# Kernel optimization log

Measured on AMD Instinct MI355X. Metric: run time of the kernel, lower is better.

Reference implementation:

```python
import jax, jax.numpy as jnp
import numpy as np
from jax import lax

PATCH = 16
TAU = 0.5
EPS = 1e-8  # torch CosineSimilarity default eps


def setup_inputs() -> dict:
    key = jax.random.key(0)
    k1, k2, k3, k4, k5 = jax.random.split(key, 5)
    B, C, HW = 64, 3, 384
    hidden, latent = 768, 1024
    return {
        "x": jax.random.normal(k1, (B, C, HW, HW), dtype=jnp.float32),
        "conv_w": jax.random.normal(k2, (hidden, C, PATCH, PATCH), dtype=jnp.float32) * 0.02,
        "conv_b": jax.random.normal(k3, (hidden,), dtype=jnp.float32) * 0.02,
        "latent1": jax.random.normal(k4, (1, latent, hidden), dtype=jnp.float32),
        "latent2": jax.random.normal(k5, (1, latent, hidden), dtype=jnp.float32),
    }


def _cosine_scores(p, p_norm, lat):
    # p: (B, N, D); lat: (L, D) -> (B, N, L) cosine similarity
    l_norm = jnp.linalg.norm(lat, axis=-1)  # (L,)
    dots = jnp.einsum('bnd,ld->bnl', p, lat)
    denom = jnp.maximum(p_norm[:, :, None] * l_norm[None, None, :], EPS)
    return dots / denom


def reference(x, conv_w, conv_b, latent1, latent2):
    # Patch embedding: Conv2d(kernel=stride=16, padding=0)
    patch = lax.conv_general_dilated(
        x, conv_w, window_strides=(PATCH, PATCH), padding='VALID',
        dimension_numbers=('NCHW', 'OIHW', 'NCHW'))
    patch = patch + conv_b[None, :, None, None]  # (B, D, H', W')
    B, D = patch.shape[0], patch.shape[1]
    p = patch.reshape(B, D, -1).transpose(0, 2, 1)  # (B, N, D)
    p_norm = jnp.linalg.norm(p, axis=-1)  # (B, N)

    far = _cosine_scores(p, p_norm, latent1[0])    # (B, N, L)
    close = _cosine_scores(p, p_norm, latent2[0])  # (B, N, L)

    sum_close = jnp.sum(jnp.exp(close / TAU), axis=(1, 2))  # (B,)
    sum_far = jnp.sum(jnp.exp(far / TAU), axis=(1, 2))      # (B,)
    loss = -jnp.log(sum_close / sum_far)
    return loss.mean()
```

## Files before the change

kernel.cpp:

```cpp
#include <hip/hip_runtime.h>
#include <math.h>

using f32x4  = __attribute__((ext_vector_type(4))) float;
using bf16x8 = __attribute__((ext_vector_type(8))) short;

typedef const __attribute__((address_space(1))) void gas_void;
typedef __attribute__((address_space(3))) void las_void;

__device__ __forceinline__ void gl16(const void* g, void* l) {
    __builtin_amdgcn_global_load_lds((gas_void*)g, (las_void*)l, 16, 0, 0);
}

__device__ __forceinline__ unsigned short f2bf(float f) {
    union { float f; unsigned u; } v; v.f = f;
    unsigned r = v.u + 0x7fffu + ((v.u >> 16) & 1u);
    return (unsigned short)(r >> 16);
}
__device__ __forceinline__ float bf2f(unsigned short u) {
    return __uint_as_float(((unsigned)u) << 16);
}

#define VW0() asm volatile("s_waitcnt vmcnt(0)")
#define VWL0() asm volatile("s_waitcnt vmcnt(0) lgkmcnt(0)")
#define BAR() __builtin_amdgcn_s_barrier()

__global__ void pcl_prep_wl(const float* __restrict__ w,
                            const float* __restrict__ l1, const float* __restrict__ l2,
                            unsigned short* __restrict__ wsW,
                            unsigned short* __restrict__ wsL) {
    int r = blockIdx.x, t = threadIdx.x;
    if (r < 768) {
        const float* src = w + (size_t)r * 768;
        unsigned short* dst = wsW + (size_t)r * 768;
#pragma unroll
        for (int i = 0; i < 12; ++i) dst[t + 64 * i] = f2bf(src[t + 64 * i]);
    } else {
        int lr = r - 768;
        const float* src = (lr < 1024) ? l1 + (size_t)lr * 768 : l2 + (size_t)(lr - 1024) * 768;
        unsigned short* dst = wsL + (size_t)lr * 768;
        float vals[12];
        float s = 0.f;
#pragma unroll
        for (int i = 0; i < 12; ++i) {
            float f = bf2f(f2bf(src[t + 64 * i]));
            vals[i] = f; s += f * f;
        }
#pragma unroll
        for (int off = 32; off; off >>= 1) s += __shfl_xor(s, off, 64);
        float rn = 1.0f / sqrtf(s);
#pragma unroll
        for (int i = 0; i < 12; ++i) dst[t + 64 * i] = f2bf(vals[i] * rn);
    }
}

#define K1_LDS 81920

__global__ __launch_bounds__(256, 2)
void pcl_k1(const float* __restrict__ x,
            const unsigned short* __restrict__ wsW,
            const float* __restrict__ bias,
            unsigned short* __restrict__ pbuf,
            float* __restrict__ rpnp) {
    extern __shared__ char smem[];
    const int t = threadIdx.x, w = t >> 6, l = t & 63;
    const int wg = (blockIdx.x & 7) * 144 + (blockIdx.x >> 3);
    const int mt = wg / 6, nt = wg % 6;
    const size_t Mb = (size_t)mt * 192;
    const int Nb = nt * 128;
    const int wm = w >> 1, wn = w & 1;
    const int ir = l >> 3, s2 = (l & 7) ^ ir;
    const int lm = l & 15, lg4 = l >> 4;

    char* buf0 = smem;
    char* buf1 = smem + 40960;

    const int sl8 = t & 7;
    const float* xbase[6];
    int awoff[6];
#pragma unroll
    for (int rep = 0; rep < 6; ++rep) {
        int row = rep * 32 + (t >> 3);
        int n = (int)Mb + row;
        int b = n / 576, n5 = n % 576;
        int ph = n5 / 24, pw = n5 % 24;
        xbase[rep] = x + (size_t)b * 442368 + (size_t)ph * 6144 + pw * 16;
        awoff[rep] = row * 128 + ((sl8 ^ (row & 7)) << 4);
    }
    auto xoff = [&](int kt) {
        int k0 = kt * 64 + sl8 * 8;
        return (k0 >> 8) * 147456 + (((k0 >> 4) & 15)) * 384 + (k0 & 15);
    };

    auto issueB = [&](int kt, char* buf) {
#pragma unroll
        for (int rr = 0; rr < 4; ++rr) {
            int c2 = w * 4 + rr;
            gl16(wsW + (size_t)(Nb + c2 * 8 + ir) * 768 + kt * 64 + s2 * 8,
                 buf + 24576 + c2 * 1024);
        }
    };

    f32x4 xr[6][2];
    auto loadX = [&](int kt) {
        int off = xoff(kt);
#pragma unroll
        for (int rep = 0; rep < 6; ++rep) {
            const float* s = xbase[rep] + off;
            xr[rep][0] = *(const f32x4*)s;
            xr[rep][1] = *(const f32x4*)(s + 4);
        }
    };
    auto writeA = [&](char* buf) {
#pragma unroll
        for (int rep = 0; rep < 6; ++rep) {
            bf16x8 pkt;
#pragma unroll
            for (int j = 0; j < 4; ++j) {
                pkt[j]     = (short)f2bf(xr[rep][0][j]);
                pkt[4 + j] = (short)f2bf(xr[rep][1][j]);
            }
            *(bf16x8*)(buf + awoff[rep]) = pkt;
        }
    };

    f32x4 acc[6][4];
#pragma unroll
    for (int m = 0; m < 6; ++m)
#pragma unroll
        for (int nb = 0; nb < 4; ++nb) acc[m][nb] = (f32x4)0.f;

    loadX(0);
    issueB(0, buf0);
    writeA(buf0);
    VWL0(); BAR();

    bf16x8 areg[3][2], breg[4][2];

#pragma unroll 2
    for (int kt = 0; kt < 12; ++kt) {
        char* cur = (kt & 1) ? buf1 : buf0;
        char* nxt = (kt & 1) ? buf0 : buf1;

        if (kt < 11) { loadX(kt + 1); issueB(kt + 1, nxt); }

#pragma unroll
        for (int nb = 0; nb < 4; ++nb)
#pragma unroll
            for (int ks = 0; ks < 2; ++ks) {
                int rb = wn * 64 + nb * 16 + lm, slot = ks * 4 + lg4;
                breg[nb][ks] = *(const bf16x8*)(cur + 24576 + rb * 128 + ((slot ^ (rb & 7)) << 4));
            }
#pragma unroll
        for (int m = 0; m < 3; ++m)
#pragma unroll
            for (int ks = 0; ks < 2; ++ks) {
                int r = wm * 96 + m * 16 + lm, slot = ks * 4 + lg4;
                areg[m][ks] = *(const bf16x8*)(cur + r * 128 + ((slot ^ (r & 7)) << 4));
            }
        __builtin_amdgcn_s_setprio(1);
#pragma unroll
        for (int m = 0; m < 3; ++m)
#pragma unroll
            for (int nb = 0; nb < 4; ++nb)
#pragma unroll
                for (int ks = 0; ks < 2; ++ks)
                    acc[m][nb] = __builtin_amdgcn_mfma_f32_16x16x32_bf16(areg[m][ks], breg[nb][ks], acc[m][nb], 0, 0, 0);
        __builtin_amdgcn_s_setprio(0);

#pragma unroll
        for (int m = 0; m < 3; ++m)
#pragma unroll
            for (int ks = 0; ks < 2; ++ks) {
                int r = wm * 96 + 48 + m * 16 + lm, slot = ks * 4 + lg4;
                areg[m][ks] = *(const bf16x8*)(cur + r * 128 + ((slot ^ (r & 7)) << 4));
            }
        __builtin_amdgcn_s_setprio(1);
#pragma unroll
        for (int m = 0; m < 3; ++m)
#pragma unroll
            for (int nb = 0; nb < 4; ++nb)
#pragma unroll
                for (int ks = 0; ks < 2; ++ks)
                    acc[3 + m][nb] = __builtin_amdgcn_mfma_f32_16x16x32_bf16(areg[m][ks], breg[nb][ks], acc[3 + m][nb], 0, 0, 0);
        __builtin_amdgcn_s_setprio(0);

        if (kt < 11) writeA(nxt);

        VWL0();
        BAR();
    }

    float rs[6][4];
#pragma unroll
    for (int m = 0; m < 6; ++m)
#pragma unroll
        for (int j = 0; j < 4; ++j) rs[m][j] = 0.f;
#pragma unroll
    for (int nb = 0; nb < 4; ++nb) {
        int d = Nb + wn * 64 + nb * 16 + lm;
        float bv = bias[d];
#pragma unroll
        for (int m = 0; m < 6; ++m) {
            int mh = m / 3, mi = m % 3;
#pragma unroll
            for (int j = 0; j < 4; ++j) {
                int row = wm * 96 + mh * 48 + mi * 16 + lg4 * 4 + j;
                unsigned short h = f2bf(acc[m][nb][j] + bv);
                pbuf[(Mb + row) * 768 + d] = h;
                float fv = bf2f(h);
                rs[m][j] += fv * fv;
            }
        }
    }
#pragma unroll
    for (int m = 0; m < 6; ++m)
#pragma unroll
        for (int j = 0; j < 4; ++j) {
            rs[m][j] += __shfl_xor(rs[m][j], 1);
            rs[m][j] += __shfl_xor(rs[m][j], 2);
            rs[m][j] += __shfl_xor(rs[m][j], 4);
            rs[m][j] += __shfl_xor(rs[m][j], 8);
        }
    __syncthreads();
    float* nrm = (float*)smem;
    if (lm == 0) {
#pragma unroll
        for (int m = 0; m < 6; ++m) {
            int mh = m / 3, mi = m % 3;
#pragma unroll
            for (int j = 0; j < 4; ++j) {
                int row = wm * 96 + mh * 48 + mi * 16 + lg4 * 4 + j;
                nrm[row * 2 + wn] = rs[m][j];
            }
        }
    }
    __syncthreads();
    if (t < 192) rpnp[(size_t)nt * 36864 + Mb + t] = nrm[t * 2] + nrm[t * 2 + 1];
}

__global__ void pcl_norm(const float* __restrict__ rpnp, float* __restrict__ rpn) {
    int i = blockIdx.x * 256 + threadIdx.x;
    float s = 0.f;
#pragma unroll
    for (int nt = 0; nt < 6; ++nt) s += rpnp[(size_t)nt * 36864 + i];
    rpn[i] = 1.0f / sqrtf(s);
}

#define K2_LDS 81920

__global__ __launch_bounds__(256, 2)
void pcl_k2(const unsigned short* __restrict__ pbuf,
            const unsigned short* __restrict__ wsL,
            const float* __restrict__ rpn,
            double* __restrict__ partials) {
    extern __shared__ char smem[];
    const int t = threadIdx.x, w = t >> 6, l = t & 63;
    const int wg = (blockIdx.x & 7) * 384 + (blockIdx.x >> 3);
    const int mt = wg >> 4, nt = wg & 15;
    const size_t Mb = (size_t)mt * 192;
    const int Nb = nt * 128;
    const int wm = w >> 1, wn = w & 1;
    const int ir = l >> 3, s2 = (l & 7) ^ ir;
    const int lm = l & 15, lg4 = l >> 4;

    char* buf0 = smem;
    char* buf1 = smem + 40960;

    auto stage = [&](int kt, char* buf) {
#pragma unroll
        for (int rr = 0; rr < 6; ++rr) {
            int c2 = w * 6 + rr;
            gl16(pbuf + (Mb + c2 * 8 + ir) * 768 + kt * 64 + s2 * 8, buf + c2 * 1024);
        }
#pragma unroll
        for (int rr = 0; rr < 4; ++rr) {
            int c2 = w * 4 + rr;
            gl16(wsL + (size_t)(Nb + c2 * 8 + ir) * 768 + kt * 64 + s2 * 8,
                 buf + 24576 + c2 * 1024);
        }
    };

    f32x4 acc[6][4];
#pragma unroll
    for (int m = 0; m < 6; ++m)
#pragma unroll
        for (int nb = 0; nb < 4; ++nb) acc[m][nb] = (f32x4)0.f;

    stage(0, buf0);
    VW0(); BAR();

    bf16x8 areg[3][2], breg[4][2];

#pragma unroll 2
    for (int kt = 0; kt < 12; ++kt) {
        char* cur = (kt & 1) ? buf1 : buf0;
        char* nxt = (kt & 1) ? buf0 : buf1;

        if (kt < 11) stage(kt + 1, nxt);

#pragma unroll
        for (int nb = 0; nb < 4; ++nb)
#pragma unroll
            for (int ks = 0; ks < 2; ++ks) {
                int rb = wn * 64 + nb * 16 + lm, slot = ks * 4 + lg4;
                breg[nb][ks] = *(const bf16x8*)(cur + 24576 + rb * 128 + ((slot ^ (rb & 7)) << 4));
            }
#pragma unroll
        for (int m = 0; m < 3; ++m)
#pragma unroll
            for (int ks = 0; ks < 2; ++ks) {
                int r = wm * 96 + m * 16 + lm, slot = ks * 4 + lg4;
                areg[m][ks] = *(const bf16x8*)(cur + r * 128 + ((slot ^ (r & 7)) << 4));
            }
        __builtin_amdgcn_s_setprio(1);
#pragma unroll
        for (int m = 0; m < 3; ++m)
#pragma unroll
            for (int nb = 0; nb < 4; ++nb)
#pragma unroll
                for (int ks = 0; ks < 2; ++ks)
                    acc[m][nb] = __builtin_amdgcn_mfma_f32_16x16x32_bf16(areg[m][ks], breg[nb][ks], acc[m][nb], 0, 0, 0);
        __builtin_amdgcn_s_setprio(0);

#pragma unroll
        for (int m = 0; m < 3; ++m)
#pragma unroll
            for (int ks = 0; ks < 2; ++ks) {
                int r = wm * 96 + 48 + m * 16 + lm, slot = ks * 4 + lg4;
                areg[m][ks] = *(const bf16x8*)(cur + r * 128 + ((slot ^ (r & 7)) << 4));
            }
        __builtin_amdgcn_s_setprio(1);
#pragma unroll
        for (int m = 0; m < 3; ++m)
#pragma unroll
            for (int nb = 0; nb < 4; ++nb)
#pragma unroll
                for (int ks = 0; ks < 2; ++ks)
                    acc[3 + m][nb] = __builtin_amdgcn_mfma_f32_16x16x32_bf16(areg[m][ks], breg[nb][ks], acc[3 + m][nb], 0, 0, 0);
        __builtin_amdgcn_s_setprio(0);

        VW0();
        BAR();
    }

    double ssum = 0.0;
#pragma unroll
    for (int m = 0; m < 6; ++m) {
        int mh = m / 3, mi = m % 3;
        int rl = wm * 96 + mh * 48 + mi * 16;
        float rv[4];
#pragma unroll
        for (int j = 0; j < 4; ++j) rv[j] = rpn[Mb + rl + lg4 * 4 + j];
        float es = 0.f;
#pragma unroll
        for (int nb = 0; nb < 4; ++nb)
#pragma unroll
            for (int j = 0; j < 4; ++j)
                es += __expf(2.0f * acc[m][nb][j] * rv[j]);
        ssum += (double)es;
    }
#pragma unroll
    for (int off = 32; off; off >>= 1) ssum += __shfl_down(ssum, off);
    __syncthreads();
    double* red = (double*)smem;
    if (l == 0) red[w] = ssum;
    __syncthreads();
    if (t == 0) {
        double s = 0.0;
#pragma unroll
        for (int i = 0; i < 4; ++i) s += red[i];
        partials[wg] = s;
    }
}

__global__ void pcl_finish(const double* __restrict__ partials, float* __restrict__ out) {
    int b = threadIdx.x;
    double far = 0.0, close = 0.0;
#pragma unroll
    for (int i = 0; i < 3; ++i) {
        int mt = b * 3 + i;
#pragma unroll
        for (int nTile = 0; nTile < 16; ++nTile) {
            double v = partials[mt * 16 + nTile];
            if (nTile < 8) far += v; else close += v;
        }
    }
    double lb = log(far) - log(close);
#pragma unroll
    for (int off = 32; off; off >>= 1) lb += __shfl_down(lb, off);
    if (b == 0) out[0] = (float)(lb * (1.0 / 64.0));
}

extern "C" void kernel_launch(void* const* d_in, const int* in_sizes, int n_in,
                              void* d_out, int out_size, void* d_ws, size_t ws_size,
                              hipStream_t stream) {
    const float* x    = (const float*)d_in[0];
    const float* w    = (const float*)d_in[1];
    const float* bias = (const float*)d_in[2];
    const float* l1   = (const float*)d_in[3];
    const float* l2   = (const float*)d_in[4];
    float* out = (float*)d_out;

    unsigned short* pbuf = (unsigned short*)d_ws;
    unsigned short* wsW  = (unsigned short*)((char*)d_ws + 56623104);
    unsigned short* wsL  = (unsigned short*)((char*)d_ws + 57802752);
    float* rpnp          = (float*)((char*)d_ws + 60948480);
    float* rpn           = (float*)((char*)d_ws + 61833216);
    double* partials     = (double*)((char*)d_ws + 61980672);

    (void)hipFuncSetAttribute((const void*)pcl_k1,
                              hipFuncAttributeMaxDynamicSharedMemorySize, K1_LDS);
    (void)hipFuncSetAttribute((const void*)pcl_k2,
                              hipFuncAttributeMaxDynamicSharedMemorySize, K2_LDS);

    pcl_prep_wl<<<2816, 64, 0, stream>>>(w, l1, l2, wsW, wsL);
    pcl_k1<<<1152, 256, K1_LDS, stream>>>(x, wsW, bias, pbuf, rpnp);
    pcl_norm<<<144, 256, 0, stream>>>(rpnp, rpn);
    pcl_k2<<<3072, 256, K2_LDS, stream>>>(pbuf, wsL, rpn, partials);
    pcl_finish<<<1, 64, 0, stream>>>(partials, out);
}
```

Before: 209.9 us.

## Pre-convert image patches to bf16 and stage both GEMM operands via async LDS loads

Adds a separate kernel that gathers each 16x16x3 patch from x, converts it to bf16 and writes it into a contiguous patch matrix. The patch-embedding GEMM then loads A as well as B with direct global-to-LDS loads, removing register staging and the in-loop conversion. The N tile also shrinks from 128 to 96, giving 8 column tiles and more workgroups. In exchange it adds an extra pass that writes and rereads about 56 MB of bf16 patches, plus one more kernel launch.

```diff
diff --git a/kernel.cpp b/kernel.cpp
--- a/kernel.cpp
+++ b/kernel.cpp
@@ -21,8 +21,26 @@
 }
 
 #define VW0() asm volatile("s_waitcnt vmcnt(0)")
-#define VWL0() asm volatile("s_waitcnt vmcnt(0) lgkmcnt(0)")
 #define BAR() __builtin_amdgcn_s_barrier()
+
+__global__ void pcl_prep_x(const float* __restrict__ x, unsigned short* __restrict__ xp) {
+    int t = threadIdx.x;
+    int wv = t >> 6, l = t & 63;
+    int p = blockIdx.x * 4 + wv;
+    int b = p / 576, n = p % 576;
+    int ph = n / 24, pw = n % 24;
+    const float* base = x + ((size_t)(b * 3)) * 147456 + (ph * 16) * 384 + pw * 16;
+    unsigned* dst = (unsigned*)(xp + (size_t)p * 768);
+#pragma unroll
+    for (int q = 0; q < 6; ++q) {
+        int k = q * 128 + l * 2;
+        int c = k >> 8, i = (k >> 4) & 15, j = k & 15;
+        const float* s = base + (size_t)c * 147456 + i * 384 + j;
+        float2 v = *(const float2*)s;
+        unsigned lo = f2bf(v.x), hi = f2bf(v.y);
+        dst[q * 64 + l] = lo | (hi << 16);
+    }
+}
 
 __global__ void pcl_prep_wl(const float* __restrict__ w,
                             const float* __restrict__ l1, const float* __restrict__ l2,
@@ -56,17 +74,17 @@
 #define K1_LDS 81920
 
 __global__ __launch_bounds__(256, 2)
-void pcl_k1(const float* __restrict__ x,
+void pcl_k1(const unsigned short* __restrict__ xp,
             const unsigned short* __restrict__ wsW,
             const float* __restrict__ bias,
             unsigned short* __restrict__ pbuf,
             float* __restrict__ rpnp) {
     extern __shared__ char smem[];
     const int t = threadIdx.x, w = t >> 6, l = t & 63;
-    const int wg = (blockIdx.x & 7) * 144 + (blockIdx.x >> 3);
-    const int mt = wg / 6, nt = wg % 6;
+    const int wg = (blockIdx.x & 7) * 192 + (blockIdx.x >> 3);
+    const int mt = wg >> 3, nt = wg & 7;
     const size_t Mb = (size_t)mt * 192;
-    const int Nb = nt * 128;
+    const int Nb = nt * 96;
     const int wm = w >> 1, wn = w & 1;
     const int ir = l >> 3, s2 = (l & 7) ^ ir;
     const int lm = l & 15, lg4 = l >> 4;
@@ -74,80 +92,43 @@
     char* buf0 = smem;
     char* buf1 = smem + 40960;
 
-    const int sl8 = t & 7;
-    const float* xbase[6];
-    int awoff[6];
-#pragma unroll
-    for (int rep = 0; rep < 6; ++rep) {
-        int row = rep * 32 + (t >> 3);
-        int n = (int)Mb + row;
-        int b = n / 576, n5 = n % 576;
-        int ph = n5 / 24, pw = n5 % 24;
-        xbase[rep] = x + (size_t)b * 442368 + (size_t)ph * 6144 + pw * 16;
-        awoff[rep] = row * 128 + ((sl8 ^ (row & 7)) << 4);
-    }
-    auto xoff = [&](int kt) {
-        int k0 = kt * 64 + sl8 * 8;
-        return (k0 >> 8) * 147456 + (((k0 >> 4) & 15)) * 384 + (k0 & 15);
-    };
-
-    auto issueB = [&](int kt, char* buf) {
-#pragma unroll
-        for (int rr = 0; rr < 4; ++rr) {
-            int c2 = w * 4 + rr;
+    auto stage = [&](int kt, char* buf) {
+#pragma unroll
+        for (int rr = 0; rr < 6; ++rr) {
+            int c2 = w * 6 + rr;
+            gl16(xp + (Mb + c2 * 8 + ir) * 768 + kt * 64 + s2 * 8, buf + c2 * 1024);
+        }
+#pragma unroll
+        for (int rr = 0; rr < 3; ++rr) {
+            int c2 = w * 3 + rr;
             gl16(wsW + (size_t)(Nb + c2 * 8 + ir) * 768 + kt * 64 + s2 * 8,
                  buf + 24576 + c2 * 1024);
         }
     };
 
-    f32x4 xr[6][2];
-    auto loadX = [&](int kt) {
-        int off = xoff(kt);
-#pragma unroll
-        for (int rep = 0; rep < 6; ++rep) {
-            const float* s = xbase[rep] + off;
-            xr[rep][0] = *(const f32x4*)s;
-            xr[rep][1] = *(const f32x4*)(s + 4);
-        }
-    };
-    auto writeA = [&](char* buf) {
-#pragma unroll
-        for (int rep = 0; rep < 6; ++rep) {
-            bf16x8 pkt;
-#pragma unroll
-            for (int j = 0; j < 4; ++j) {
-                pkt[j]     = (short)f2bf(xr[rep][0][j]);
-                pkt[4 + j] = (short)f2bf(xr[rep][1][j]);
-            }
-            *(bf16x8*)(buf + awoff[rep]) = pkt;
-        }
-    };
-
-    f32x4 acc[6][4];
+    f32x4 acc[6][3];
 #pragma unroll
     for (int m = 0; m < 6; ++m)
 #pragma unroll
-        for (int nb = 0; nb < 4; ++nb) acc[m][nb] = (f32x4)0.f;
-
-    loadX(0);
-    issueB(0, buf0);
-    writeA(buf0);
-    VWL0(); BAR();
-
-    bf16x8 areg[3][2], breg[4][2];
+        for (int nb = 0; nb < 3; ++nb) acc[m][nb] = (f32x4)0.f;
+
+    stage(0, buf0);
+    VW0(); BAR();
+
+    bf16x8 areg[3][2], breg[3][2];
 
 #pragma unroll 2
     for (int kt = 0; kt < 12; ++kt) {
         char* cur = (kt & 1) ? buf1 : buf0;
         char* nxt = (kt & 1) ? buf0 : buf1;
 
-        if (kt < 11) { loadX(kt + 1); issueB(kt + 1, nxt); }
-
-#pragma unroll
-        for (int nb = 0; nb < 4; ++nb)
-#pragma unroll
-            for (int ks = 0; ks < 2; ++ks) {
-                int rb = wn * 64 + nb * 16 + lm, slot = ks * 4 + lg4;
+        if (kt < 11) stage(kt + 1, nxt);
+
+#pragma unroll
+        for (int nb = 0; nb < 3; ++nb)
+#pragma unroll
+            for (int ks = 0; ks < 2; ++ks) {
+                int rb = wn * 48 + nb * 16 + lm, slot = ks * 4 + lg4;
                 breg[nb][ks] = *(const bf16x8*)(cur + 24576 + rb * 128 + ((slot ^ (rb & 7)) << 4));
             }
 #pragma unroll
@@ -161,7 +142,7 @@
 #pragma unroll
         for (int m = 0; m < 3; ++m)
 #pragma unroll
-            for (int nb = 0; nb < 4; ++nb)
+            for (int nb = 0; nb < 3; ++nb)
 #pragma unroll
                 for (int ks = 0; ks < 2; ++ks)
                     acc[m][nb] = __builtin_amdgcn_mfma_f32_16x16x32_bf16(areg[m][ks], breg[nb][ks], acc[m][nb], 0, 0, 0);
@@ -178,15 +159,13 @@
 #pragma unroll
         for (int m = 0; m < 3; ++m)
 #pragma unroll
-            for (int nb = 0; nb < 4; ++nb)
+            for (int nb = 0; nb < 3; ++nb)
 #pragma unroll
                 for (int ks = 0; ks < 2; ++ks)
                     acc[3 + m][nb] = __builtin_amdgcn_mfma_f32_16x16x32_bf16(areg[m][ks], breg[nb][ks], acc[3 + m][nb], 0, 0, 0);
         __builtin_amdgcn_s_setprio(0);
 
-        if (kt < 11) writeA(nxt);
-
-        VWL0();
+        VW0();
         BAR();
     }
 
@@ -196,8 +175,8 @@
 #pragma unroll
         for (int j = 0; j < 4; ++j) rs[m][j] = 0.f;
 #pragma unroll
-    for (int nb = 0; nb < 4; ++nb) {
-        int d = Nb + wn * 64 + nb * 16 + lm;
+    for (int nb = 0; nb < 3; ++nb) {
+        int d = Nb + wn * 48 + nb * 16 + lm;
         float bv = bias[d];
 #pragma unroll
         for (int m = 0; m < 6; ++m) {
@@ -242,7 +221,7 @@
     int i = blockIdx.x * 256 + threadIdx.x;
     float s = 0.f;
 #pragma unroll
-    for (int nt = 0; nt < 6; ++nt) s += rpnp[(size_t)nt * 36864 + i];
+    for (int nt = 0; nt < 8; ++nt) s += rpnp[(size_t)nt * 36864 + i];
     rpn[i] = 1.0f / sqrtf(s);
 }
 
@@ -401,20 +380,22 @@
     const float* l2   = (const float*)d_in[4];
     float* out = (float*)d_out;
 
-    unsigned short* pbuf = (unsigned short*)d_ws;
-    unsigned short* wsW  = (unsigned short*)((char*)d_ws + 56623104);
-    unsigned short* wsL  = (unsigned short*)((char*)d_ws + 57802752);
-    float* rpnp          = (float*)((char*)d_ws + 60948480);
-    float* rpn           = (float*)((char*)d_ws + 61833216);
-    double* partials     = (double*)((char*)d_ws + 61980672);
+    unsigned short* xp   = (unsigned short*)d_ws;
+    unsigned short* pbuf = (unsigned short*)((char*)d_ws + 56623104);
+    unsigned short* wsW  = (unsigned short*)((char*)d_ws + 113246208);
+    unsigned short* wsL  = (unsigned short*)((char*)d_ws + 114425856);
+    float* rpnp          = (float*)((char*)d_ws + 117571584);
+    float* rpn           = (float*)((char*)d_ws + 118751232);
+    double* partials     = (double*)((char*)d_ws + 118898688);
 
     (void)hipFuncSetAttribute((const void*)pcl_k1,
                               hipFuncAttributeMaxDynamicSharedMemorySize, K1_LDS);
     (void)hipFuncSetAttribute((const void*)pcl_k2,
                               hipFuncAttributeMaxDynamicSharedMemorySize, K2_LDS);
 
+    pcl_prep_x<<<9216, 256, 0, stream>>>(x, xp);
     pcl_prep_wl<<<2816, 64, 0, stream>>>(w, l1, l2, wsW, wsL);
-    pcl_k1<<<1152, 256, K1_LDS, stream>>>(x, wsW, bias, pbuf, rpnp);
+    pcl_k1<<<1536, 256, K1_LDS, stream>>>(xp, wsW, bias, pbuf, rpnp);
     pcl_norm<<<144, 256, 0, stream>>>(rpnp, rpn);
     pcl_k2<<<3072, 256, K2_LDS, stream>>>(pbuf, wsL, rpn, partials);
     pcl_finish<<<1, 64, 0, stream>>>(partials, out);
```

New measurement: 194.8 us. 1.08x faster.
